# Performance work log

Hardware: AMD Instinct MI355X
Metric: run time of the kernel (lower is better)

## Reference

```python
import jax, jax.numpy as jnp
import numpy as np

K = 5  # kernel_size per dim, dim=2 -> 25 kernel weights, degree-1 open B-splines


def _spline_basis(pseudo):
    """Degree-1 open B-spline basis for dim=2, kernel_size=5.
    pseudo: [E,2] in [0,1]. Returns basis [E,4], kernel index wi [E,4]."""
    v = pseudo * (K - 1)                      # [E,2]
    lo = jnp.floor(v)
    frac = v - lo                             # [E,2]
    lo = lo.astype(jnp.int32)
    b = jnp.stack([1.0 - frac, frac], axis=-1)            # [E,2,2] (edge, dim, offset)
    idx = jnp.clip(lo[..., None] + jnp.arange(2, dtype=jnp.int32), 0, K - 1)  # [E,2,2]
    basis = b[:, 0, :, None] * b[:, 1, None, :]           # [E,2,2]
    wi = idx[:, 0, :, None] + K * idx[:, 1, None, :]      # [E,2,2] (dim0 stride 1, dim1 stride K)
    E = pseudo.shape[0]
    return basis.reshape(E, 4), wi.reshape(E, 4)


def _spline_conv(x, src, dst, pseudo, W, root, bias, num_nodes):
    basis, wi = _spline_basis(pseudo)          # [E,4], [E,4]
    xW = jnp.einsum('ni,kio->nko', x, W)       # [N,25,out]
    gathered = xW[src[:, None], wi]            # [E,4,out]
    msg = jnp.einsum('es,eso->eo', basis, gathered)  # [E,out]
    agg = jax.ops.segment_max(msg, dst, num_segments=num_nodes)
    agg = jnp.where(jnp.isneginf(agg), 0.0, agg)  # empty segments -> 0 (PyG fill)
    return agg + x @ root + bias


def setup_inputs() -> dict:
    key = jax.random.key(0)
    ks = jax.random.split(key, 12)
    N, E, C = 50000, 800000, 64
    s = 1.0 / np.sqrt(C)
    return {
        'x': jax.random.normal(ks[0], (N, C), jnp.float32),
        'edge_index': jax.random.randint(ks[1], (2, E), 0, N, jnp.int32),
        'edge_attr': jax.random.uniform(ks[2], (E, 2), jnp.float32),
        'W1': jax.random.normal(ks[3], (25, C, C), jnp.float32) * s,
        'root1': jax.random.normal(ks[4], (C, C), jnp.float32) * s,
        'b1': jnp.zeros((C,), jnp.float32),
        'W2': jax.random.normal(ks[5], (25, C, C), jnp.float32) * s,
        'root2': jax.random.normal(ks[6], (C, C), jnp.float32) * s,
        'b2': jnp.zeros((C,), jnp.float32),
        'final_w': jax.random.normal(ks[7], (3 * C, C), jnp.float32) / np.sqrt(3 * C),
        'final_b': jnp.zeros((C,), jnp.float32),
    }


def reference(x, edge_index, edge_attr, W1, root1, b1, W2, root2, b2, final_w, final_b):
    N = x.shape[0]
    src, dst = edge_index[0], edge_index[1]
    x1 = jax.nn.relu(_spline_conv(x, src, dst, edge_attr, W1, root1, b1, N))
    x2 = jax.nn.relu(_spline_conv(x1, src, dst, edge_attr, W2, root2, b2, N))
    h = jnp.concatenate([x, x1, x2], axis=-1)   # cat=True; dropout p=0 (eval)
    return h @ final_w + final_b
```

## Files before the change

### kernel.cpp

```cpp
#include <hip/hip_runtime.h>
#include <hip/hip_bf16.h>


typedef short  bf16x8 __attribute__((ext_vector_type(8)));
typedef float  f32x4  __attribute__((ext_vector_type(4)));

__device__ __forceinline__ float bf2f(ushort u) {
    return __uint_as_float((uint)u << 16);
}
__device__ __forceinline__ ushort f2bf(float f) {
    uint u = __float_as_uint(f);
    return (ushort)((u + 0x7FFF + ((u >> 16) & 1)) >> 16);
}

__global__ __launch_bounds__(256) void cvt_f32_bf16(
    const float* __restrict__ in, ushort* __restrict__ out, int n)
{
    int i = blockIdx.x * 256 + threadIdx.x;
    if (i < n) out[i] = f2bf(in[i]);
}

__global__ __launch_bounds__(256) void cvt_WT(
    const float* __restrict__ W, const float* __restrict__ root,
    ushort* __restrict__ Wt)
{
    int idx = blockIdx.x * 256 + threadIdx.x;
    if (idx >= 26 * 4096) return;
    int tile = idx >> 12, rem = idx & 4095, o = rem >> 6, i = rem & 63;
    float v = (tile < 25) ? W[tile * 4096 + i * 64 + o] : root[i * 64 + o];
    Wt[idx] = f2bf(v);
}

__global__ __launch_bounds__(256) void zero_ints(int* __restrict__ p, int n)
{
    int i = blockIdx.x * 256 + threadIdx.x;
    if (i < n) p[i] = 0;
}

__global__ __launch_bounds__(256) void hist_deg(
    const int* __restrict__ ei, int* __restrict__ deg, int E)
{
    int e = blockIdx.x * 256 + threadIdx.x;
    if (e < E) atomicAdd(&deg[ei[E + e]], 1);
}

__global__ __launch_bounds__(1024) void scan_block(
    const int* __restrict__ deg, int* __restrict__ inc,
    int* __restrict__ partial, int N)
{
    __shared__ int s[1024];
    int i = blockIdx.x * 1024 + threadIdx.x;
    int v = (i < N) ? deg[i] : 0;
    s[threadIdx.x] = v;
    __syncthreads();
    for (int off = 1; off < 1024; off <<= 1) {
        int t = (threadIdx.x >= off) ? s[threadIdx.x - off] : 0;
        __syncthreads();
        s[threadIdx.x] += t;
        __syncthreads();
    }
    if (i < N) inc[i] = s[threadIdx.x];
    if (threadIdx.x == 1023) partial[blockIdx.x] = s[1023];
}

__global__ void scan_partial(int* __restrict__ partial, int nb)
{
    __shared__ int s[64];
    int t = threadIdx.x;
    int v = (t < nb) ? partial[t] : 0;
    s[t] = v;
    __syncthreads();
    for (int off = 1; off < 64; off <<= 1) {
        int x = (t >= off) ? s[t - off] : 0;
        __syncthreads();
        s[t] += x;
        __syncthreads();
    }
    if (t < nb) partial[t] = s[t] - v;
}

__global__ __launch_bounds__(1024) void scan_finalize(
    const int* __restrict__ deg, const int* __restrict__ inc,
    const int* __restrict__ partial, int* __restrict__ row_ptr,
    int* __restrict__ cursor, int N)
{
    int i = blockIdx.x * 1024 + threadIdx.x;
    if (i >= N) return;
    int v = inc[i] + partial[blockIdx.x];
    row_ptr[i + 1] = v;
    cursor[i] = v - deg[i];
    if (i == 0) row_ptr[0] = 0;
}

__global__ __launch_bounds__(256) void gemm_scatter(
    const ushort* __restrict__ A, const ushort* __restrict__ Wt,
    ushort* __restrict__ xWb, float* __restrict__ xRoot, int mtiles,
    const int* __restrict__ ei, const float* __restrict__ attr,
    int* __restrict__ cursor, int4* __restrict__ epack, int E)
{
    __shared__ ushort Cs[64][72];
    const int bx = blockIdx.x;

    if (bx >= 26) {
        if (!ei) return;
        int e = ((bx - 26) * gridDim.y + blockIdx.y) * 256 + threadIdx.x;
        if (e >= E) return;
        int src = ei[e], dst = ei[E + e];
        float u = attr[2 * e] * 4.f;
        float v = attr[2 * e + 1] * 4.f;
        float lu = floorf(u), lv = floorf(v);
        float fu = u - lu, fv = v - lv;
        int iu = (int)lu;  iu = iu < 0 ? 0 : (iu > 4 ? 4 : iu);
        int iv = (int)lv;  iv = iv < 0 ? 0 : (iv > 4 ? 4 : iv);
        int iu1 = iu + 1 > 4 ? 4 : iu + 1;
        int iv1 = iv + 1 > 4 ? 4 : iv + 1;
        uint slots = (uint)(iu + 5 * iv) | ((uint)(iu + 5 * iv1) << 8) |
                     ((uint)(iu1 + 5 * iv) << 16) | ((uint)(iu1 + 5 * iv1) << 24);
        uint wlo = (uint)f2bf((1.f - fu) * (1.f - fv)) | ((uint)f2bf((1.f - fu) * fv) << 16);
        uint whi = (uint)f2bf(fu * (1.f - fv)) | ((uint)f2bf(fu * fv) << 16);
        int pos = atomicAdd(&cursor[dst], 1);
        epack[pos] = make_int4(src * 3200, (int)slots, (int)wlo, (int)whi);
        return;
    }

    const int wave = threadIdx.x >> 6;
    const int lane = threadIdx.x & 63;
    const int l16 = lane & 15;
    const int half = lane >> 4;
    const int tid = threadIdx.x;

    const ushort* btile = Wt + (size_t)bx * 4096;
    bf16x8 b0[4], b1[4];
    #pragma unroll
    for (int s = 0; s < 4; ++s) {
        const ushort* brow = btile + (size_t)(s * 16 + l16) * 64;
        b0[s] = *(const bf16x8*)(brow + half * 8);
        b1[s] = *(const bf16x8*)(brow + 32 + half * 8);
    }

    for (int it = 0; it < 8; ++it) {
        const int mt = blockIdx.y * 8 + it;
        if (mt >= mtiles) break;
        const int m0 = mt * 64;
        const int m_base = m0 + wave * 16;

        const ushort* arow = A + (size_t)(m_base + l16) * 64;
        bf16x8 a0 = *(const bf16x8*)(arow + half * 8);
        bf16x8 a1 = *(const bf16x8*)(arow + 32 + half * 8);

        f32x4 acc[4];
        #pragma unroll
        for (int s = 0; s < 4; ++s) {
            acc[s] = (f32x4){0.f, 0.f, 0.f, 0.f};
            acc[s] = __builtin_amdgcn_mfma_f32_16x16x32_bf16(a0, b0[s], acc[s], 0, 0, 0);
            acc[s] = __builtin_amdgcn_mfma_f32_16x16x32_bf16(a1, b1[s], acc[s], 0, 0, 0);
        }

        if (bx == 25) {
            #pragma unroll
            for (int s = 0; s < 4; ++s)
                #pragma unroll
                for (int r = 0; r < 4; ++r)
                    xRoot[(size_t)(m_base + half * 4 + r) * 64 + s * 16 + l16] = acc[s][r];
            continue;
        }

        #pragma unroll
        for (int s = 0; s < 4; ++s)
            #pragma unroll
            for (int r = 0; r < 4; ++r)
                Cs[wave * 16 + half * 4 + r][s * 16 + l16] = f2bf(acc[s][r]);
        __syncthreads();
        #pragma unroll
        for (int i2 = 0; i2 < 2; ++i2) {
            int idx = tid + i2 * 256;
            int row = idx >> 3, seg = idx & 7;
            uint4 v = *(const uint4*)&Cs[row][seg * 8];
            *(uint4*)(xWb + (size_t)(m0 + row) * 1600 + bx * 64 + seg * 8) = v;
        }
        __syncthreads();
    }
}

__device__ __forceinline__ void gather4(
    const char* __restrict__ xwb, int lane, int rb, uint slots, ushort g[4])
{
    g[0] = *((const ushort*)(xwb + rb + ((slots & 255u) << 7)) + lane);
    g[1] = *((const ushort*)(xwb + rb + (((slots >> 8) & 255u) << 7)) + lane);
    g[2] = *((const ushort*)(xwb + rb + (((slots >> 16) & 255u) << 7)) + lane);
    g[3] = *((const ushort*)(xwb + rb + ((slots >> 24) << 7)) + lane);
}

__device__ __forceinline__ float consume4(const int4 d, const ushort g[4])
{
    float m = __uint_as_float((uint)d.z << 16) * bf2f(g[0]);
    m = fmaf(__uint_as_float((uint)d.z & 0xffff0000u), bf2f(g[1]), m);
    m = fmaf(__uint_as_float((uint)d.w << 16), bf2f(g[2]), m);
    m = fmaf(__uint_as_float((uint)d.w & 0xffff0000u), bf2f(g[3]), m);
    return m;
}

__global__ __launch_bounds__(256) void edge_csr(
    const ushort* __restrict__ xWb, const int* __restrict__ row_ptr,
    const int4* __restrict__ epack, const float* __restrict__ xRoot,
    const float* __restrict__ bias, float* __restrict__ outf,
    ushort* __restrict__ outb, int N)
{
    const int wv = __builtin_amdgcn_readfirstlane(threadIdx.x >> 6);
    const int d = blockIdx.x * 4 + wv;
    const int lane = threadIdx.x & 63;
    if (d >= N) return;
    const int e0 = __builtin_amdgcn_readfirstlane(row_ptr[d]);
    const int e1 = __builtin_amdgcn_readfirstlane(row_ptr[d + 1]);
    const char* xwb = (const char*)xWb;

    float vmax = -__builtin_inff();
    int e = e0;
    const int pairs = (e1 - e0) >> 1;
    if (pairs > 0) {
        int4 dA = epack[e], dB = epack[e + 1];
        ushort gA[4], gB[4];
        gather4(xwb, lane, dA.x, (uint)dA.y, gA);
        gather4(xwb, lane, dB.x, (uint)dB.y, gB);
        for (int p = 1; p < pairs; ++p) {
            int4 nA = epack[e + 2 * p], nB = epack[e + 2 * p + 1];
            ushort hA[4], hB[4];
            gather4(xwb, lane, nA.x, (uint)nA.y, hA);
            gather4(xwb, lane, nB.x, (uint)nB.y, hB);
            vmax = fmaxf(vmax, fmaxf(consume4(dA, gA), consume4(dB, gB)));
            #pragma unroll
            for (int i = 0; i < 4; ++i) { gA[i] = hA[i]; gB[i] = hB[i]; }
            dA = nA; dB = nB;
        }
        vmax = fmaxf(vmax, fmaxf(consume4(dA, gA), consume4(dB, gB)));
        e += pairs * 2;
    }
    if (e < e1) {
        int4 dA = epack[e];
        ushort gA[4];
        gather4(xwb, lane, dA.x, (uint)dA.y, gA);
        vmax = fmaxf(vmax, consume4(dA, gA));
    }
    if (e1 == e0) vmax = 0.f;
    float val = vmax + xRoot[(size_t)d * 64 + lane] + bias[lane];
    val = fmaxf(val, 0.f);
    outf[(size_t)d * 64 + lane] = val;
    if (outb) outb[(size_t)d * 64 + lane] = f2bf(val);
}

__global__ __launch_bounds__(256) void final_gemm(
    const float* __restrict__ x, const float* __restrict__ x1,
    const float* __restrict__ x2, const float* __restrict__ fw,
    const float* __restrict__ fb, float* __restrict__ out, int M)
{
    __shared__ float As[64][68];
    __shared__ float Bs[64][68];
    const int m0 = blockIdx.x * 64;
    const int tid = threadIdx.x;
    const int tx = tid & 15, ty = tid >> 4;
    float acc[4][4] = {};
    const float* srcs[3] = {x, x1, x2};

    for (int kt = 0; kt < 3; ++kt) {
        const float* A = srcs[kt];
        const float4* B4 = (const float4*)(fw + (size_t)kt * 4096);
        #pragma unroll
        for (int r = 0; r < 4; ++r) {
            int idx = tid + r * 256;
            float4 v = B4[idx];
            int i = idx >> 4;
            int o = (idx & 15) * 4;
            Bs[i][o] = v.x; Bs[i][o + 1] = v.y; Bs[i][o + 2] = v.z; Bs[i][o + 3] = v.w;
        }
        #pragma unroll
        for (int r = 0; r < 4; ++r) {
            int idx = tid + r * 256;
            int m = idx >> 4;
            int k = (idx & 15) * 4;
            int gm = m0 + m;
            float4 v = make_float4(0.f, 0.f, 0.f, 0.f);
            if (gm < M) v = *(const float4*)(A + (size_t)gm * 64 + k);
            As[k][m] = v.x; As[k + 1][m] = v.y; As[k + 2][m] = v.z; As[k + 3][m] = v.w;
        }
        __syncthreads();
        #pragma unroll 8
        for (int k = 0; k < 64; ++k) {
            float4 av = *(const float4*)&As[k][ty * 4];
            float4 bv = *(const float4*)&Bs[k][tx * 4];
            float aa[4] = {av.x, av.y, av.z, av.w};
            float bb[4] = {bv.x, bv.y, bv.z, bv.w};
            #pragma unroll
            for (int i = 0; i < 4; ++i)
                #pragma unroll
                for (int j = 0; j < 4; ++j)
                    acc[i][j] = fmaf(aa[i], bb[j], acc[i][j]);
        }
        __syncthreads();
    }

    #pragma unroll
    for (int i = 0; i < 4; ++i) {
        int gm = m0 + ty * 4 + i;
        if (gm < M) {
            float4 v = make_float4(acc[i][0] + fb[tx * 4 + 0],
                                   acc[i][1] + fb[tx * 4 + 1],
                                   acc[i][2] + fb[tx * 4 + 2],
                                   acc[i][3] + fb[tx * 4 + 3]);
            *(float4*)(out + (size_t)gm * 64 + tx * 4) = v;
        }
    }
}

extern "C" void kernel_launch(void* const* d_in, const int* in_sizes, int n_in,
                              void* d_out, int out_size, void* d_ws, size_t ws_size,
                              hipStream_t stream)
{
    const float* x    = (const float*)d_in[0];
    const int*   ei   = (const int*)d_in[1];
    const float* attr = (const float*)d_in[2];
    const float* W1   = (const float*)d_in[3];
    const float* r1   = (const float*)d_in[4];
    const float* b1   = (const float*)d_in[5];
    const float* W2   = (const float*)d_in[6];
    const float* r2   = (const float*)d_in[7];
    const float* b2   = (const float*)d_in[8];
    const float* fw   = (const float*)d_in[9];
    const float* fb   = (const float*)d_in[10];
    float* out = (float*)d_out;

    const int N = in_sizes[0] / 64;
    const int E = in_sizes[1] / 2;
    const int mtiles = (N + 63) / 64;
    const int Npad = mtiles * 64;

    char* p = (char*)d_ws;
    auto alloc = [&](size_t bytes) { void* q = p; p += (bytes + 255) & ~(size_t)255; return q; };
    int4*   epack  = (int4*)alloc((size_t)E * 16);
    float*  x1f    = (float*)alloc((size_t)Npad * 64 * 4);
    float*  x2f    = (float*)alloc((size_t)Npad * 64 * 4);
    float*  xRoot  = (float*)alloc((size_t)Npad * 64 * 4);
    ushort* xWb    = (ushort*)alloc((size_t)Npad * 1600 * 2);
    ushort* xb     = (ushort*)alloc((size_t)Npad * 64 * 2);
    ushort* x1b    = (ushort*)alloc((size_t)Npad * 64 * 2);
    ushort* WtA    = (ushort*)alloc((size_t)26 * 4096 * 2);
    ushort* WtB    = (ushort*)alloc((size_t)26 * 4096 * 2);
    int*    deg    = (int*)alloc((size_t)N * 4);
    int*    cursor = (int*)alloc((size_t)N * 4);
    int*    rowp   = (int*)alloc((size_t)(N + 1) * 4);
    int*    tmpinc = (int*)alloc((size_t)N * 4);
    int*    part   = (int*)alloc(64 * 4);

    const int nb = (N + 1023) / 1024;

    cvt_f32_bf16<<<(N * 64 + 255) / 256, 256, 0, stream>>>(x, xb, N * 64);
    cvt_WT<<<(26 * 4096 + 255) / 256, 256, 0, stream>>>(W1, r1, WtA);
    cvt_WT<<<(26 * 4096 + 255) / 256, 256, 0, stream>>>(W2, r2, WtB);

    zero_ints<<<(N + 255) / 256, 256, 0, stream>>>(deg, N);
    hist_deg<<<(E + 255) / 256, 256, 0, stream>>>(ei, deg, E);
    scan_block<<<nb, 1024, 0, stream>>>(deg, tmpinc, part, N);
    scan_partial<<<1, 64, 0, stream>>>(part, nb);
    scan_finalize<<<nb, 1024, 0, stream>>>(deg, tmpinc, part, rowp, cursor, N);

    const int gy = (mtiles + 7) / 8;
    const int sc_blocks = (E + 255) / 256;
    const int sc_cols = (sc_blocks + gy - 1) / gy;

    gemm_scatter<<<dim3(26 + sc_cols, gy), 256, 0, stream>>>(
        xb, WtA, xWb, xRoot, mtiles, ei, attr, cursor, epack, E);
    edge_csr<<<(N + 3) / 4, 256, 0, stream>>>(xWb, rowp, epack, xRoot, b1, x1f, x1b, N);

    gemm_scatter<<<dim3(26, gy), 256, 0, stream>>>(
        x1b, WtB, xWb, xRoot, mtiles, nullptr, nullptr, nullptr, nullptr, E);
    edge_csr<<<(N + 3) / 4, 256, 0, stream>>>(xWb, rowp, epack, xRoot, b2, x2f, nullptr, N);

    final_gemm<<<mtiles, 256, 0, stream>>>(x, x1f, x2f, fw, fb, out, N);
}
```

Before: 422.5 us.

## Use bf16 MFMA for final GEMM and fuse prep conversion kernels

Measured after the change: 420.3 us. About the same (-0.5%).

```diff
diff --git a/kernel.cpp b/kernel.cpp
--- a/kernel.cpp
+++ b/kernel.cpp
@@ -13,28 +13,36 @@
     return (ushort)((u + 0x7FFF + ((u >> 16) & 1)) >> 16);
 }
 
-__global__ __launch_bounds__(256) void cvt_f32_bf16(
-    const float* __restrict__ in, ushort* __restrict__ out, int n)
-{
-    int i = blockIdx.x * 256 + threadIdx.x;
-    if (i < n) out[i] = f2bf(in[i]);
-}
-
-__global__ __launch_bounds__(256) void cvt_WT(
-    const float* __restrict__ W, const float* __restrict__ root,
-    ushort* __restrict__ Wt)
-{
+__global__ __launch_bounds__(256) void prep(
+    const float* __restrict__ x, ushort* __restrict__ xb, int nx,
+    const float* __restrict__ W1, const float* __restrict__ r1, ushort* __restrict__ WtA,
+    const float* __restrict__ W2, const float* __restrict__ r2, ushort* __restrict__ WtB,
+    const float* __restrict__ fw, ushort* __restrict__ fwT,
+    int* __restrict__ deg, int N)
+{
+    const int nw = 26 * 4096, nfw = 3 * 4096;
     int idx = blockIdx.x * 256 + threadIdx.x;
-    if (idx >= 26 * 4096) return;
-    int tile = idx >> 12, rem = idx & 4095, o = rem >> 6, i = rem & 63;
-    float v = (tile < 25) ? W[tile * 4096 + i * 64 + o] : root[i * 64 + o];
-    Wt[idx] = f2bf(v);
-}
-
-__global__ __launch_bounds__(256) void zero_ints(int* __restrict__ p, int n)
-{
-    int i = blockIdx.x * 256 + threadIdx.x;
-    if (i < n) p[i] = 0;
+    if (idx < nx) { xb[idx] = f2bf(x[idx]); return; }
+    idx -= nx;
+    if (idx < nw) {
+        int tile = idx >> 12, rem = idx & 4095, o = rem >> 6, i = rem & 63;
+        WtA[idx] = f2bf(tile < 25 ? W1[tile * 4096 + i * 64 + o] : r1[i * 64 + o]);
+        return;
+    }
+    idx -= nw;
+    if (idx < nw) {
+        int tile = idx >> 12, rem = idx & 4095, o = rem >> 6, i = rem & 63;
+        WtB[idx] = f2bf(tile < 25 ? W2[tile * 4096 + i * 64 + o] : r2[i * 64 + o]);
+        return;
+    }
+    idx -= nw;
+    if (idx < nfw) {
+        int t = idx >> 12, rem = idx & 4095, o = rem >> 6, k = rem & 63;
+        fwT[idx] = f2bf(fw[(t * 64 + k) * 64 + o]);
+        return;
+    }
+    idx -= nfw;
+    if (idx < N) deg[idx] = 0;
 }
 
 __global__ __launch_bounds__(256) void hist_deg(
@@ -244,69 +252,50 @@
     if (e1 == e0) vmax = 0.f;
     float val = vmax + xRoot[(size_t)d * 64 + lane] + bias[lane];
     val = fmaxf(val, 0.f);
-    outf[(size_t)d * 64 + lane] = val;
+    if (outf) outf[(size_t)d * 64 + lane] = val;
     if (outb) outb[(size_t)d * 64 + lane] = f2bf(val);
 }
 
-__global__ __launch_bounds__(256) void final_gemm(
-    const float* __restrict__ x, const float* __restrict__ x1,
-    const float* __restrict__ x2, const float* __restrict__ fw,
+__global__ __launch_bounds__(256) void final_mfma(
+    const ushort* __restrict__ xb, const ushort* __restrict__ x1b,
+    const ushort* __restrict__ x2b, const ushort* __restrict__ fwT,
     const float* __restrict__ fb, float* __restrict__ out, int M)
 {
-    __shared__ float As[64][68];
-    __shared__ float Bs[64][68];
-    const int m0 = blockIdx.x * 64;
-    const int tid = threadIdx.x;
-    const int tx = tid & 15, ty = tid >> 4;
-    float acc[4][4] = {};
-    const float* srcs[3] = {x, x1, x2};
-
-    for (int kt = 0; kt < 3; ++kt) {
-        const float* A = srcs[kt];
-        const float4* B4 = (const float4*)(fw + (size_t)kt * 4096);
+    const int wave = threadIdx.x >> 6;
+    const int lane = threadIdx.x & 63;
+    const int l16 = lane & 15;
+    const int half = lane >> 4;
+    const int m_base = blockIdx.x * 64 + wave * 16;
+    const ushort* srcs[3] = {xb, x1b, x2b};
+
+    f32x4 acc[4];
+    #pragma unroll
+    for (int s = 0; s < 4; ++s) acc[s] = (f32x4){0.f, 0.f, 0.f, 0.f};
+
+    #pragma unroll
+    for (int t = 0; t < 3; ++t) {
+        const ushort* arow = srcs[t] + (size_t)(m_base + l16) * 64;
+        bf16x8 a0 = *(const bf16x8*)(arow + half * 8);
+        bf16x8 a1 = *(const bf16x8*)(arow + 32 + half * 8);
+        const ushort* btile = fwT + (size_t)t * 4096;
+        #pragma unroll
+        for (int s = 0; s < 4; ++s) {
+            const ushort* brow = btile + (size_t)(s * 16 + l16) * 64;
+            bf16x8 b0 = *(const bf16x8*)(brow + half * 8);
+            bf16x8 b1 = *(const bf16x8*)(brow + 32 + half * 8);
+            acc[s] = __builtin_amdgcn_mfma_f32_16x16x32_bf16(a0, b0, acc[s], 0, 0, 0);
+            acc[s] = __builtin_amdgcn_mfma_f32_16x16x32_bf16(a1, b1, acc[s], 0, 0, 0);
+        }
+    }
+
+    #pragma unroll
+    for (int s = 0; s < 4; ++s) {
+        int o = s * 16 + l16;
+        float b = fb[o];
         #pragma unroll
         for (int r = 0; r < 4; ++r) {
-            int idx = tid + r * 256;
-            float4 v = B4[idx];
-            int i = idx >> 4;
-            int o = (idx & 15) * 4;
-            Bs[i][o] = v.x; Bs[i][o + 1] = v.y; Bs[i][o + 2] = v.z; Bs[i][o + 3] = v.w;
-        }
-        #pragma unroll
-        for (int r = 0; r < 4; ++r) {
-            int idx = tid + r * 256;
-            int m = idx >> 4;
-            int k = (idx & 15) * 4;
-            int gm = m0 + m;
-            float4 v = make_float4(0.f, 0.f, 0.f, 0.f);
-            if (gm < M) v = *(const float4*)(A + (size_t)gm * 64 + k);
-            As[k][m] = v.x; As[k + 1][m] = v.y; As[k + 2][m] = v.z; As[k + 3][m] = v.w;
-        }
-        __syncthreads();
-        #pragma unroll 8
-        for (int k = 0; k < 64; ++k) {
-            float4 av = *(const float4*)&As[k][ty * 4];
-            float4 bv = *(const float4*)&Bs[k][tx * 4];
-            float aa[4] = {av.x, av.y, av.z, av.w};
-            float bb[4] = {bv.x, bv.y, bv.z, bv.w};
-            #pragma unroll
-            for (int i = 0; i < 4; ++i)
-                #pragma unroll
-                for (int j = 0; j < 4; ++j)
-                    acc[i][j] = fmaf(aa[i], bb[j], acc[i][j]);
-        }
-        __syncthreads();
-    }
-
-    #pragma unroll
-    for (int i = 0; i < 4; ++i) {
-        int gm = m0 + ty * 4 + i;
-        if (gm < M) {
-            float4 v = make_float4(acc[i][0] + fb[tx * 4 + 0],
-                                   acc[i][1] + fb[tx * 4 + 1],
-                                   acc[i][2] + fb[tx * 4 + 2],
-                                   acc[i][3] + fb[tx * 4 + 3]);
-            *(float4*)(out + (size_t)gm * 64 + tx * 4) = v;
+            int m = m_base + half * 4 + r;
+            if (m < M) out[(size_t)m * 64 + o] = acc[s][r] + b;
         }
     }
 }
@@ -337,13 +326,14 @@
     auto alloc = [&](size_t bytes) { void* q = p; p += (bytes + 255) & ~(size_t)255; return q; };
     int4*   epack  = (int4*)alloc((size_t)E * 16);
     float*  x1f    = (float*)alloc((size_t)Npad * 64 * 4);
-    float*  x2f    = (float*)alloc((size_t)Npad * 64 * 4);
     float*  xRoot  = (float*)alloc((size_t)Npad * 64 * 4);
     ushort* xWb    = (ushort*)alloc((size_t)Npad * 1600 * 2);
     ushort* xb     = (ushort*)alloc((size_t)Npad * 64 * 2);
     ushort* x1b    = (ushort*)alloc((size_t)Npad * 64 * 2);
+    ushort* x2b    = (ushort*)alloc((size_t)Npad * 64 * 2);
     ushort* WtA    = (ushort*)alloc((size_t)26 * 4096 * 2);
     ushort* WtB    = (ushort*)alloc((size_t)26 * 4096 * 2);
+    ushort* fwT    = (ushort*)alloc((size_t)3 * 4096 * 2);
     int*    deg    = (int*)alloc((size_t)N * 4);
     int*    cursor = (int*)alloc((size_t)N * 4);
     int*    rowp   = (int*)alloc((size_t)(N + 1) * 4);
@@ -352,11 +342,10 @@
 
     const int nb = (N + 1023) / 1024;
 
-    cvt_f32_bf16<<<(N * 64 + 255) / 256, 256, 0, stream>>>(x, xb, N * 64);
-    cvt_WT<<<(26 * 4096 + 255) / 256, 256, 0, stream>>>(W1, r1, WtA);
-    cvt_WT<<<(26 * 4096 + 255) / 256, 256, 0, stream>>>(W2, r2, WtB);
-
-    zero_ints<<<(N + 255) / 256, 256, 0, stream>>>(deg, N);
+    const int nprep = N * 64 + 2 * 26 * 4096 + 3 * 4096 + N;
+    prep<<<(nprep + 255) / 256, 256, 0, stream>>>(
+        x, xb, N * 64, W1, r1, WtA, W2, r2, WtB, fw, fwT, deg, N);
+
     hist_deg<<<(E + 255) / 256, 256, 0, stream>>>(ei, deg, E);
     scan_block<<<nb, 1024, 0, stream>>>(deg, tmpinc, part, N);
     scan_partial<<<1, 64, 0, stream>>>(part, nb);
@@ -372,7 +361,7 @@
 
     gemm_scatter<<<dim3(26, gy), 256, 0, stream>>>(
         x1b, WtB, xWb, xRoot, mtiles, nullptr, nullptr, nullptr, nullptr, E);
-    edge_csr<<<(N + 3) / 4, 256, 0, stream>>>(xWb, rowp, epack, xRoot, b2, x2f, nullptr, N);
-
-    final_gemm<<<mtiles, 256, 0, stream>>>(x, x1f, x2f, fw, fb, out, N);
-}
+    edge_csr<<<(N + 3) / 4, 256, 0, stream>>>(xWb, rowp, epack, xRoot, b2, nullptr, x2b, N);
+
+    final_mfma<<<mtiles, 256, 0, stream>>>(xb, x1b, x2b, fwT, fb, out, N);
+}
```
